# Optimization experiments

Hardware: AMD Instinct MI355X
Metric: run time of the kernel (lower is better)

## Reference

```python
import jax, jax.numpy as jnp
import numpy as np

K_MAX = 3
ITERS = 3
NEG_BIG = -1e9


def squash(x):
    # x: [..., O]
    sn = jnp.sum(jnp.square(x), axis=-1, keepdims=True)
    factor = sn / (1.0 + sn) / jnp.sqrt(sn + 1e-8)
    return factor * x


def setup_inputs() -> dict:
    key = jax.random.key(0)
    k1, k2, k3, k4 = jax.random.split(key, 4)
    N, L, D, O = 4096, 200, 64, 64
    behavior_embs = jax.random.normal(k1, (N, L, D), dtype=jnp.float32)
    W = jax.random.normal(k2, (D, O), dtype=jnp.float32)  # init_std=1.0
    routing_logits_init = jax.random.normal(k3, (N, K_MAX, L), dtype=jnp.float32)
    seq_len = jax.random.randint(k4, (N, 1), 0, L, dtype=jnp.int32)
    return {
        "behavior_embs": behavior_embs,
        "W": W,
        "routing_logits_init": routing_logits_init,
        "seq_len": seq_len,
    }


def reference(behavior_embs, W, routing_logits_init, seq_len):
    N, L, D = behavior_embs.shape
    # mask: [N, K_MAX, L] -- valid positions along L, tiled across capsules
    mask = jnp.arange(L)[None, None, :] < seq_len[:, None, :]  # [N,1,L]
    mask = jnp.broadcast_to(mask, (N, K_MAX, L))

    mappings = jnp.matmul(behavior_embs, W)          # [N, L, O]
    m_det = jax.lax.stop_gradient(mappings)         # routing uses detached mappings

    logits = routing_logits_init                     # [N, K_MAX, L]
    for _ in range(ITERS - 1):
        padded = jnp.where(mask, logits, NEG_BIG)
        # NOTE: softmax over the capsule dim (axis=1), as in the original
        weights = jax.nn.softmax(padded, axis=1)     # [N, K_MAX, L]
        candidates = jnp.matmul(weights, m_det)      # [N, K_MAX, O]
        interests = squash(candidates)
        logits = logits + jnp.einsum('nko,nlo->nkl', interests, m_det)

    padded = jnp.where(mask, logits, NEG_BIG)
    weights = jax.nn.softmax(padded, axis=1)
    candidates = jnp.matmul(weights, mappings)       # final iter uses non-detached
    interests = squash(candidates)                   # [N, K_MAX, O]
    return interests
```

## Files before the change

kernel.cpp:

```cpp
#include <hip/hip_runtime.h>
#include <math.h>

typedef _Float16 f16;
typedef _Float16 f16x8 __attribute__((ext_vector_type(8)));
typedef float f32x4 __attribute__((ext_vector_type(4)));

#define LSEQ 200
#define LT 13
#define LKS 7

__global__ __launch_bounds__(256, 4)
void capsule_kernel(const float* __restrict__ E,
                    const float* __restrict__ W,
                    const float* __restrict__ RL,
                    const int* __restrict__ SL,
                    float* __restrict__ out)
{
    __shared__ f16 m_sw[LT*2*64*8];
    __shared__ f16 w_sw[LKS*64*8];
    __shared__ f16 i_sw[2*64*8];
    __shared__ float logits[3*LSEQ];
    __shared__ float cand[3*64];

    const int n = blockIdx.x;
    const int t = threadIdx.x;
    const int lane = t & 63;
    const int wv = t >> 6;
    const int q = lane >> 4;
    const int cc = lane & 15;

    const int o_own = wv*16 + cc;
    float wf[16];
    #pragma unroll
    for (int ks = 0; ks < 2; ks++)
        #pragma unroll
        for (int j = 0; j < 8; j++)
            wf[ks*8 + j] = W[(ks*32 + q*8 + j)*64 + o_own];

    const float4 f4z = make_float4(0.f, 0.f, 0.f, 0.f);
    for (int g = t; g < 448; g += 256) *(float4*)&w_sw[g*8] = f4z;
    for (int g = t; g < 128; g += 256) *(float4*)&i_sw[g*8] = f4z;

    const float* Eb = E + (size_t)n * (LSEQ*64);
    for (int g = t; g < LT*2*64; g += 256) {
        int sb = g >> 6, c = g & 63;
        int Tl = sb >> 1, ks = sb & 1;
        int qq = c >> 4, m = c & 15;
        int l = Tl*16 + m;
        int kb = ks*32 + qq*8;
        float4 v0 = f4z, v1 = f4z;
        if (l < LSEQ) {
            v0 = *(const float4*)(Eb + l*64 + kb);
            v1 = *(const float4*)(Eb + l*64 + kb + 4);
        }
        f16x8 h = { (f16)v0.x,(f16)v0.y,(f16)v0.z,(f16)v0.w,
                    (f16)v1.x,(f16)v1.y,(f16)v1.z,(f16)v1.w };
        *(f16x8*)&m_sw[g*8] = h;
    }

    if (t < LSEQ) {
        const float* R = RL + (size_t)n * (3*LSEQ);
        logits[t]          = R[t];
        logits[LSEQ + t]   = R[LSEQ + t];
        logits[2*LSEQ + t] = R[2*LSEQ + t];
    }
    const int s = SL[n];

    __syncthreads();

    f16x8 wB[2];
    #pragma unroll
    for (int ks = 0; ks < 2; ks++) {
        f16x8 h;
        #pragma unroll
        for (int j = 0; j < 8; j++) h[j] = (f16)wf[ks*8 + j];
        wB[ks] = h;
    }
    f32x4 acc[LT];
    #pragma unroll
    for (int Tl = 0; Tl < LT; Tl++) {
        f32x4 c0 = {0.f, 0.f, 0.f, 0.f};
        #pragma unroll
        for (int ks = 0; ks < 2; ks++) {
            f16x8 a = *(f16x8*)&m_sw[((Tl*2 + ks)*64 + lane)*8];
            c0 = __builtin_amdgcn_mfma_f32_16x16x32_f16(a, wB[ks], c0, 0, 0, 0);
        }
        acc[Tl] = c0;
    }
    __syncthreads();

    const int kso = o_own >> 5, qo = (o_own & 31) >> 3, jo = o_own & 7;
    #pragma unroll
    for (int Tl = 0; Tl < LT; Tl++) {
        #pragma unroll
        for (int r = 0; r < 4; r++) {
            int lp = q*4 + r;
            m_sw[((Tl*2 + kso)*64 + qo*16 + lp)*8 + jo] = (f16)acc[Tl][r];
        }
    }
    __syncthreads();

    f16x8 mfrag[LKS];
    #pragma unroll
    for (int ks = 0; ks < LKS; ks++) {
        f16x8 h;
        #pragma unroll
        for (int j = 0; j < 8; j++) {
            int l = ks*32 + q*8 + j;
            f16 v = (f16)0.f;
            if (l < 208) {
                int Tl = l >> 4, lp = l & 15;
                v = m_sw[((Tl*2 + kso)*64 + qo*16 + lp)*8 + jo];
            }
            h[j] = v;
        }
        mfrag[ks] = h;
    }

    for (int iter = 0; iter < 3; iter++) {
        if (t < LSEQ) {
            float w0, w1, w2;
            if (t < s) {
                float l0 = logits[t], l1 = logits[LSEQ + t], l2 = logits[2*LSEQ + t];
                float mx = fmaxf(fmaxf(l0, l1), l2);
                float e0 = expf(l0 - mx), e1 = expf(l1 - mx), e2 = expf(l2 - mx);
                float inv = 1.f / (e0 + e1 + e2);
                w0 = e0*inv; w1 = e1*inv; w2 = e2*inv;
            } else {
                w0 = w1 = w2 = (1.f/3.f);
            }
            int ks = t >> 5, qq = (t & 31) >> 3, j = t & 7;
            int base = (ks*64 + qq*16)*8 + j;
            w_sw[base]      = (f16)w0;
            w_sw[base + 8]  = (f16)w1;
            w_sw[base + 16] = (f16)w2;
        }
        __syncthreads();

        f32x4 ca = {0.f, 0.f, 0.f, 0.f};
        #pragma unroll
        for (int ks = 0; ks < LKS; ks++) {
            f16x8 b = *(f16x8*)&w_sw[(ks*64 + lane)*8];
            ca = __builtin_amdgcn_mfma_f32_16x16x32_f16(mfrag[ks], b, ca, 0, 0, 0);
        }
        if (cc < 3) {
            #pragma unroll
            for (int r = 0; r < 4; r++) cand[cc*64 + wv*16 + q*4 + r] = ca[r];
        }
        __syncthreads();

        if (t < 192) {
            float x = cand[t];
            float sq = x*x;
            #pragma unroll
            for (int off = 32; off >= 1; off >>= 1) sq += __shfl_xor(sq, off, 64);
            float factor = sq / ((1.f + sq) * sqrtf(sq + 1e-8f));
            float y = factor * x;
            if (iter < 2) {
                int k = t >> 6, o = t & 63;
                i_sw[(((o >> 5)*4 + ((o & 31) >> 3))*16 + k)*8 + (o & 7)] = (f16)y;
            } else {
                out[(size_t)n*192 + t] = y;
            }
        }
        if (iter == 2) break;
        __syncthreads();

        for (int Tn = wv; Tn < LT; Tn += 4) {
            f32x4 da = {0.f, 0.f, 0.f, 0.f};
            #pragma unroll
            for (int ko = 0; ko < 2; ko++) {
                f16x8 a = *(f16x8*)&i_sw[(ko*64 + lane)*8];
                f16x8 b = *(f16x8*)&m_sw[((Tn*2 + ko)*64 + lane)*8];
                da = __builtin_amdgcn_mfma_f32_16x16x32_f16(a, b, da, 0, 0, 0);
            }
            if (lane < 16) {
                int l = Tn*16 + lane;
                if (l < LSEQ) {
                    logits[l]          += da[0];
                    logits[LSEQ + l]   += da[1];
                    logits[2*LSEQ + l] += da[2];
                }
            }
        }
        __syncthreads();
    }
}

extern "C" void kernel_launch(void* const* d_in, const int* in_sizes, int n_in,
                              void* d_out, int out_size, void* d_ws, size_t ws_size,
                              hipStream_t stream) {
    const float* E  = (const float*)d_in[0];
    const float* W  = (const float*)d_in[1];
    const float* RL = (const float*)d_in[2];
    const int*   SL = (const int*)d_in[3];
    float* o = (float*)d_out;
    const int N = in_sizes[3];
    capsule_kernel<<<dim3(N), dim3(256), 0, stream>>>(E, W, RL, SL, o);
}
```

Baseline: 313.4 us.

## Fuse softmax into logit update and compact weight/interest LDS buffers

Moves the per-iteration softmax into the logit-update epilogue, so new routing weights are produced right after the logits are updated. This removes one barrier and one pass over the logits per iteration. The weight and interest buffers become compact row-major arrays read with predicated loads (only lanes with cc<3 load, the rest use zeros), which drops the zero-init stores and the padded fragment layout. It also vectorizes the routing-logit load to float4 and converts W to fp16 at load time. The cost is that the softmax now runs only in lanes <16 of each wave, which serializes that work somewhat.

```diff
diff --git a/kernel.cpp b/kernel.cpp
--- a/kernel.cpp
+++ b/kernel.cpp
@@ -8,6 +8,8 @@
 #define LSEQ 200
 #define LT 13
 #define LKS 7
+#define WSTRIDE 224
+#define ISTRIDE 80
 
 __global__ __launch_bounds__(256, 4)
 void capsule_kernel(const float* __restrict__ E,
@@ -17,8 +19,8 @@
                     float* __restrict__ out)
 {
     __shared__ f16 m_sw[LT*2*64*8];
-    __shared__ f16 w_sw[LKS*64*8];
-    __shared__ f16 i_sw[2*64*8];
+    __shared__ f16 w_c[3*WSTRIDE];
+    __shared__ f16 i_c[3*ISTRIDE];
     __shared__ float logits[3*LSEQ];
     __shared__ float cand[3*64];
 
@@ -30,16 +32,16 @@
     const int cc = lane & 15;
 
     const int o_own = wv*16 + cc;
-    float wf[16];
-    #pragma unroll
-    for (int ks = 0; ks < 2; ks++)
-        #pragma unroll
-        for (int j = 0; j < 8; j++)
-            wf[ks*8 + j] = W[(ks*32 + q*8 + j)*64 + o_own];
+    f16x8 wB[2];
+    #pragma unroll
+    for (int ks = 0; ks < 2; ks++) {
+        f16x8 h;
+        #pragma unroll
+        for (int j = 0; j < 8; j++) h[j] = (f16)W[(ks*32 + q*8 + j)*64 + o_own];
+        wB[ks] = h;
+    }
 
     const float4 f4z = make_float4(0.f, 0.f, 0.f, 0.f);
-    for (int g = t; g < 448; g += 256) *(float4*)&w_sw[g*8] = f4z;
-    for (int g = t; g < 128; g += 256) *(float4*)&i_sw[g*8] = f4z;
 
     const float* Eb = E + (size_t)n * (LSEQ*64);
     for (int g = t; g < LT*2*64; g += 256) {
@@ -58,24 +60,14 @@
         *(f16x8*)&m_sw[g*8] = h;
     }
 
-    if (t < LSEQ) {
-        const float* R = RL + (size_t)n * (3*LSEQ);
-        logits[t]          = R[t];
-        logits[LSEQ + t]   = R[LSEQ + t];
-        logits[2*LSEQ + t] = R[2*LSEQ + t];
+    if (t < 150) {
+        float4 v = *(const float4*)(RL + (size_t)n * 600 + t*4);
+        *(float4*)&logits[t*4] = v;
     }
     const int s = SL[n];
 
     __syncthreads();
 
-    f16x8 wB[2];
-    #pragma unroll
-    for (int ks = 0; ks < 2; ks++) {
-        f16x8 h;
-        #pragma unroll
-        for (int j = 0; j < 8; j++) h[j] = (f16)wf[ks*8 + j];
-        wB[ks] = h;
-    }
     f32x4 acc[LT];
     #pragma unroll
     for (int Tl = 0; Tl < LT; Tl++) {
@@ -117,30 +109,32 @@
         mfrag[ks] = h;
     }
 
+    if (t < LSEQ) {
+        float w0, w1, w2;
+        if (t < s) {
+            float l0 = logits[t], l1 = logits[LSEQ + t], l2 = logits[2*LSEQ + t];
+            float mx = fmaxf(fmaxf(l0, l1), l2);
+            float e0 = expf(l0 - mx), e1 = expf(l1 - mx), e2 = expf(l2 - mx);
+            float inv = 1.f / (e0 + e1 + e2);
+            w0 = e0*inv; w1 = e1*inv; w2 = e2*inv;
+        } else {
+            w0 = w1 = w2 = (1.f/3.f);
+        }
+        w_c[t]             = (f16)w0;
+        w_c[WSTRIDE + t]   = (f16)w1;
+        w_c[2*WSTRIDE + t] = (f16)w2;
+    }
+    __syncthreads();
+
+    const f16x8 hz = {(f16)0.f,(f16)0.f,(f16)0.f,(f16)0.f,
+                      (f16)0.f,(f16)0.f,(f16)0.f,(f16)0.f};
+
     for (int iter = 0; iter < 3; iter++) {
-        if (t < LSEQ) {
-            float w0, w1, w2;
-            if (t < s) {
-                float l0 = logits[t], l1 = logits[LSEQ + t], l2 = logits[2*LSEQ + t];
-                float mx = fmaxf(fmaxf(l0, l1), l2);
-                float e0 = expf(l0 - mx), e1 = expf(l1 - mx), e2 = expf(l2 - mx);
-                float inv = 1.f / (e0 + e1 + e2);
-                w0 = e0*inv; w1 = e1*inv; w2 = e2*inv;
-            } else {
-                w0 = w1 = w2 = (1.f/3.f);
-            }
-            int ks = t >> 5, qq = (t & 31) >> 3, j = t & 7;
-            int base = (ks*64 + qq*16)*8 + j;
-            w_sw[base]      = (f16)w0;
-            w_sw[base + 8]  = (f16)w1;
-            w_sw[base + 16] = (f16)w2;
-        }
-        __syncthreads();
-
         f32x4 ca = {0.f, 0.f, 0.f, 0.f};
         #pragma unroll
         for (int ks = 0; ks < LKS; ks++) {
-            f16x8 b = *(f16x8*)&w_sw[(ks*64 + lane)*8];
+            f16x8 b = hz;
+            if (cc < 3) b = *(f16x8*)&w_c[cc*WSTRIDE + ks*32 + q*8];
             ca = __builtin_amdgcn_mfma_f32_16x16x32_f16(mfrag[ks], b, ca, 0, 0, 0);
         }
         if (cc < 3) {
@@ -158,7 +152,7 @@
             float y = factor * x;
             if (iter < 2) {
                 int k = t >> 6, o = t & 63;
-                i_sw[(((o >> 5)*4 + ((o & 31) >> 3))*16 + k)*8 + (o & 7)] = (f16)y;
+                i_c[k*ISTRIDE + o] = (f16)y;
             } else {
                 out[(size_t)n*192 + t] = y;
             }
@@ -170,16 +164,30 @@
             f32x4 da = {0.f, 0.f, 0.f, 0.f};
             #pragma unroll
             for (int ko = 0; ko < 2; ko++) {
-                f16x8 a = *(f16x8*)&i_sw[(ko*64 + lane)*8];
+                f16x8 a = hz;
+                if (cc < 3) a = *(f16x8*)&i_c[cc*ISTRIDE + ko*32 + q*8];
                 f16x8 b = *(f16x8*)&m_sw[((Tn*2 + ko)*64 + lane)*8];
                 da = __builtin_amdgcn_mfma_f32_16x16x32_f16(a, b, da, 0, 0, 0);
             }
             if (lane < 16) {
                 int l = Tn*16 + lane;
                 if (l < LSEQ) {
-                    logits[l]          += da[0];
-                    logits[LSEQ + l]   += da[1];
-                    logits[2*LSEQ + l] += da[2];
+                    float w0, w1, w2;
+                    if (l < s) {
+                        float l0 = logits[l]          + da[0];
+                        float l1 = logits[LSEQ + l]   + da[1];
+                        float l2 = logits[2*LSEQ + l] + da[2];
+                        logits[l] = l0; logits[LSEQ + l] = l1; logits[2*LSEQ + l] = l2;
+                        float mx = fmaxf(fmaxf(l0, l1), l2);
+                        float e0 = expf(l0 - mx), e1 = expf(l1 - mx), e2 = expf(l2 - mx);
+                        float inv = 1.f / (e0 + e1 + e2);
+                        w0 = e0*inv; w1 = e1*inv; w2 = e2*inv;
+                    } else {
+                        w0 = w1 = w2 = (1.f/3.f);
+                    }
+                    w_c[l]             = (f16)w0;
+                    w_c[WSTRIDE + l]   = (f16)w1;
+                    w_c[2*WSTRIDE + l] = (f16)w2;
                 }
             }
         }
```

Result: no change. 314.6 us (+0.4%).
